# Optimization experiments

Hardware: AMD Instinct MI355X
Metric: run time of the kernel (lower is better)

## Reference

```python
import jax, jax.numpy as jnp
import numpy as np

FEATURE_DIM = 4
LOSS_WEIGHT = 1.0
DELTA_V = 0.5
DELTA_D = 1.5
NUM_LABELS = 8  # instance ids 0..7; 0 = background
B, H, W = 16, 640, 640


def _safe_norm(x, axis):
    # L2 norm with grad-safe sqrt (forward value exact: 0 when sum of squares is 0)
    sq = jnp.sum(x * x, axis=axis)
    pos = sq > 0
    return jnp.where(pos, jnp.sqrt(jnp.where(pos, sq, 1.0)), 0.0)


def _single_loss(emb, instance, kernel, training_mask):
    # emb: [H,W,C], instance: [H,W] int, kernel/training_mask: [H,W] float
    C = emb.shape[-1]
    L = NUM_LABELS
    tm = training_mask > 0.5
    kr = kernel > 0.5
    inst = jnp.where(tm, instance, 0).reshape(-1)          # [P]
    inst_k = jnp.where(kr.reshape(-1), inst, 0)            # [P]
    emb_f = emb.reshape(-1, C)                              # [P,C]

    # per-label kernel-region means (emb_mean), label 0 column is zeros
    sums = jax.ops.segment_sum(emb_f, inst_k, num_segments=L)                       # [L,C]
    cnts = jax.ops.segment_sum(jnp.ones(inst_k.shape, jnp.float32), inst_k, L)      # [L]
    mu = sums / jnp.maximum(cnts, 1.0)[:, None]
    mu = mu.at[0].set(0.0)

    # aggregation term: per-pixel distance to its instance mean
    d = _safe_norm(emb_f - mu[inst], axis=1)                                         # [P]
    term = jnp.log(jnp.maximum(d - DELTA_V, 0.0) ** 2 + 1.0)
    cnt_i = jax.ops.segment_sum(jnp.ones(inst.shape, jnp.float32), inst, L)
    agg = jax.ops.segment_sum(term, inst, L) / jnp.maximum(cnt_i, 1.0)               # [L]
    # original skips label 0, then takes mean of l_agg[1:] -> drops first nonzero label
    l_agg = jnp.mean(agg[2:])

    # discrimination term: all ordered pairs of distinct nonzero labels
    dd = _safe_norm(mu[:, None, :] - mu[None, :, :], axis=-1)                        # [L,L]
    valid = (1.0 - jnp.eye(L, dtype=jnp.float32)).at[0, :].set(0.0).at[:, 0].set(0.0)
    dis = jnp.log(jnp.maximum(2.0 * DELTA_D - dd, 0.0) ** 2 + 1.0)
    l_dis = jnp.sum(dis * valid) / jnp.sum(valid)

    l_reg = jnp.mean(jnp.log(_safe_norm(mu, axis=1) + 1.0)) * 0.001
    return l_agg + l_dis + l_reg


def reference(emb, instance, kernel, training_mask):
    losses = jax.vmap(_single_loss)(emb, instance, kernel, training_mask)  # [B]
    return LOSS_WEIGHT * jnp.mean(losses)


def setup_inputs() -> dict:
    key = jax.random.key(0)
    k1, k2, k3 = jax.random.split(key, 3)
    emb = jax.random.normal(k1, (B, H, W, FEATURE_DIM), dtype=jnp.float32)
    instance = jax.random.randint(k2, (B, H, W), 0, NUM_LABELS, dtype=jnp.int32)
    kernel = jax.random.uniform(k3, (B, H, W), dtype=jnp.float32)
    training_mask = jnp.ones((B, H, W), dtype=jnp.float32)
    return {"emb": emb, "instance": instance, "kernel": kernel, "training_mask": training_mask}
```

## Files before the change

kernel.cpp:

```cpp
#include <hip/hip_runtime.h>
#include <math.h>

#define NLAB 8
#define BATCH 16
#define S_OFF  0
#define CK_OFF 28
#define CI_OFF 35
#define AG_OFF 41
#define ACC_PER_B 48
#define ACC_FLOATS (BATCH * ACC_PER_B)
#define LAB_OFFSET 4096
#define GX_ACC 64
#define GX_AGG 96
#define ILP 8

typedef __attribute__((ext_vector_type(2))) float v2f;

__device__ __forceinline__ v2f v2fma(v2f a, v2f b, v2f c) {
#if defined(__has_builtin) && __has_builtin(__builtin_elementwise_fma)
  return __builtin_elementwise_fma(a, b, c);
#else
  v2f r; r.x = fmaf(a.x, b.x, c.x); r.y = fmaf(a.y, b.y, c.y); return r;
#endif
}

__device__ __forceinline__ float wave_reduce(float v) {
#pragma unroll
  for (int off = 32; off > 0; off >>= 1) v += __shfl_xor(v, off, 64);
  return v;
}

__global__ __launch_bounds__(256, 4) void k_accum(
    const float4* __restrict__ emb, const int* __restrict__ inst,
    const float* __restrict__ ker, const float* __restrict__ tmk,
    float* __restrict__ acc, unsigned char* __restrict__ labc,
    int P, int use_cache)
{
  const int b = blockIdx.y;
  const size_t base = (size_t)b * P;
  const float4* e  = emb + base;
  const int*    ip = inst + base;
  const float*  kp = ker + base;
  const float*  tp = tmk + base;
  unsigned char* lb = labc + base;

  v2f s2[7][2], cnt2[7];
#pragma unroll
  for (int j = 0; j < 7; ++j) {
    s2[j][0] = (v2f)(0.f);
    s2[j][1] = (v2f)(0.f);
    cnt2[j]  = (v2f)(0.f);
  }

  const int T   = blockDim.x * gridDim.x;
  const int tid = blockIdx.x * blockDim.x + threadIdx.x;

  int p0 = tid;
  for (; p0 + (ILP - 1) * T < P; p0 += ILP * T) {
    int   iv[ILP]; float tv[ILP], kv[ILP]; float4 ev[ILP];
#pragma unroll
    for (int k = 0; k < ILP; ++k) iv[k] = ip[p0 + k * T];
#pragma unroll
    for (int k = 0; k < ILP; ++k) tv[k] = tp[p0 + k * T];
#pragma unroll
    for (int k = 0; k < ILP; ++k) kv[k] = kp[p0 + k * T];
#pragma unroll
    for (int k = 0; k < ILP; ++k) ev[k] = e[p0 + k * T];
    __builtin_amdgcn_sched_barrier(0);

    int lab[ILP]; float kf[ILP];
#pragma unroll
    for (int k = 0; k < ILP; ++k) {
      lab[k] = (tv[k] > 0.5f) ? (iv[k] & 7) : 0;
      kf[k]  = (kv[k] > 0.5f) ? 1.f : 0.f;
      if (use_cache) lb[p0 + k * T] = (unsigned char)lab[k];
    }

#pragma unroll
    for (int l = 1; l < NLAB; ++l) {
#pragma unroll
      for (int k = 0; k < ILP; ++k) {
        float m  = (lab[k] == l) ? 1.f : 0.f;
        float mk = m * kf[k];
        v2f mk2; mk2.x = mk; mk2.y = mk;
        v2f e01; e01.x = ev[k].x; e01.y = ev[k].y;
        v2f e23; e23.x = ev[k].z; e23.y = ev[k].w;
        v2f cm;  cm.x = mk; cm.y = m;
        s2[l - 1][0] = v2fma(mk2, e01, s2[l - 1][0]);
        s2[l - 1][1] = v2fma(mk2, e23, s2[l - 1][1]);
        cnt2[l - 1] += cm;
      }
    }
  }
  for (int p = p0; p < P; p += T) {
    int   iv = ip[p];
    float tv = tp[p];
    float kv = kp[p];
    float4 ev = e[p];
    int lab = (tv > 0.5f) ? (iv & 7) : 0;
    float kf = (kv > 0.5f) ? 1.f : 0.f;
    if (use_cache) lb[p] = (unsigned char)lab;
#pragma unroll
    for (int l = 1; l < NLAB; ++l) {
      float m  = (lab == l) ? 1.f : 0.f;
      float mk = m * kf;
      v2f mk2; mk2.x = mk; mk2.y = mk;
      v2f e01; e01.x = ev.x; e01.y = ev.y;
      v2f e23; e23.x = ev.z; e23.y = ev.w;
      v2f cm;  cm.x = mk; cm.y = m;
      s2[l - 1][0] = v2fma(mk2, e01, s2[l - 1][0]);
      s2[l - 1][1] = v2fma(mk2, e23, s2[l - 1][1]);
      cnt2[l - 1] += cm;
    }
  }

  __shared__ float red[4][48];
  const int wid = threadIdx.x >> 6, lane = threadIdx.x & 63;
#pragma unroll
  for (int j = 0; j < 7; ++j) {
    float v0 = wave_reduce(s2[j][0].x);
    float v1 = wave_reduce(s2[j][0].y);
    float v2 = wave_reduce(s2[j][1].x);
    float v3 = wave_reduce(s2[j][1].y);
    float vk = wave_reduce(cnt2[j].x);
    if (lane == 0) {
      red[wid][S_OFF + j * 4 + 0] = v0;
      red[wid][S_OFF + j * 4 + 1] = v1;
      red[wid][S_OFF + j * 4 + 2] = v2;
      red[wid][S_OFF + j * 4 + 3] = v3;
      red[wid][CK_OFF + j] = vk;
    }
    if (j >= 1) {
      float vi = wave_reduce(cnt2[j].y);
      if (lane == 0) red[wid][CI_OFF + (j - 1)] = vi;
    }
  }
  __syncthreads();
  if (threadIdx.x < AG_OFF) {
    float v = red[0][threadIdx.x] + red[1][threadIdx.x] +
              red[2][threadIdx.x] + red[3][threadIdx.x];
    atomicAdd(acc + b * ACC_PER_B + threadIdx.x, v);
  }
}

__global__ __launch_bounds__(256, 6) void k_agg(
    const float4* __restrict__ emb, const int* __restrict__ inst,
    const float* __restrict__ tmk, const unsigned char* __restrict__ labc,
    float* __restrict__ acc, int P, int use_cache)
{
  const int b = blockIdx.y;
  const size_t base = (size_t)b * P;
  __shared__ float4 smu[NLAB];
  const float* accB = acc + b * ACC_PER_B;
  if (threadIdx.x < NLAB) {
    int l = threadIdx.x;
    float4 m;
    if (l == 0) {
      m = make_float4(0.f, 0.f, 0.f, 0.f);
    } else {
      float inv = 1.f / fmaxf(accB[CK_OFF + l - 1], 1.f);
      m = make_float4(accB[S_OFF + (l - 1) * 4 + 0] * inv,
                      accB[S_OFF + (l - 1) * 4 + 1] * inv,
                      accB[S_OFF + (l - 1) * 4 + 2] * inv,
                      accB[S_OFF + (l - 1) * 4 + 3] * inv);
    }
    smu[l] = m;
  }
  __syncthreads();

  const float4* e = emb + base;
  const unsigned char* lb = labc + base;
  const int*   ip = inst + base;
  const float* tp = tmk + base;

  float aggl[6];
#pragma unroll
  for (int l = 0; l < 6; ++l) aggl[l] = 0.f;

  const int T   = blockDim.x * gridDim.x;
  const int tid = blockIdx.x * blockDim.x + threadIdx.x;

  int p0 = tid;
  for (; p0 + (ILP - 1) * T < P; p0 += ILP * T) {
    int lab[ILP]; float4 ev[ILP];
    if (use_cache) {
#pragma unroll
      for (int k = 0; k < ILP; ++k) lab[k] = lb[p0 + k * T];
    } else {
      int iv[ILP]; float tv[ILP];
#pragma unroll
      for (int k = 0; k < ILP; ++k) iv[k] = ip[p0 + k * T];
#pragma unroll
      for (int k = 0; k < ILP; ++k) tv[k] = tp[p0 + k * T];
#pragma unroll
      for (int k = 0; k < ILP; ++k) lab[k] = (tv[k] > 0.5f) ? (iv[k] & 7) : 0;
    }
#pragma unroll
    for (int k = 0; k < ILP; ++k) ev[k] = e[p0 + k * T];
    __builtin_amdgcn_sched_barrier(0);

#pragma unroll
    for (int k = 0; k < ILP; ++k) {
      float4 mv = smu[lab[k]];
      float dx = ev[k].x - mv.x, dy = ev[k].y - mv.y;
      float dz = ev[k].z - mv.z, dw = ev[k].w - mv.w;
      float sq = dx * dx + dy * dy + dz * dz + dw * dw;
      float d  = sqrtf(sq);
      float t  = fmaxf(d - 0.5f, 0.f);
      float term = (lab[k] >= 2) ? logf(fmaf(t, t, 1.f)) : 0.f;
#pragma unroll
      for (int l = 0; l < 6; ++l) aggl[l] += (lab[k] == l + 2) ? term : 0.f;
    }
  }
  for (int p = p0; p < P; p += T) {
    int lab;
    if (use_cache) lab = lb[p];
    else           lab = (tp[p] > 0.5f) ? (ip[p] & 7) : 0;
    float4 ev = e[p];
    float4 mv = smu[lab];
    float dx = ev.x - mv.x, dy = ev.y - mv.y;
    float dz = ev.z - mv.z, dw = ev.w - mv.w;
    float d = sqrtf(dx * dx + dy * dy + dz * dz + dw * dw);
    float t = fmaxf(d - 0.5f, 0.f);
    float term = (lab >= 2) ? logf(fmaf(t, t, 1.f)) : 0.f;
#pragma unroll
    for (int l = 0; l < 6; ++l) aggl[l] += (lab == l + 2) ? term : 0.f;
  }

  __shared__ float red[4][8];
  const int wid = threadIdx.x >> 6, lane = threadIdx.x & 63;
#pragma unroll
  for (int l = 0; l < 6; ++l) {
    float v = wave_reduce(aggl[l]);
    if (lane == 0) red[wid][l] = v;
  }
  __syncthreads();
  if (threadIdx.x < 6) {
    float v = red[0][threadIdx.x] + red[1][threadIdx.x] +
              red[2][threadIdx.x] + red[3][threadIdx.x];
    atomicAdd(acc + b * ACC_PER_B + AG_OFF + threadIdx.x, v);
  }
}

__global__ void k_final(const float* __restrict__ acc, float* __restrict__ out, int nb) {
  const int lane = threadIdx.x;
  float loss = 0.f;
  if (lane < nb) {
    const float* a = acc + lane * ACC_PER_B;
    float mu[NLAB][4];
#pragma unroll
    for (int c = 0; c < 4; ++c) mu[0][c] = 0.f;
#pragma unroll
    for (int l = 1; l < NLAB; ++l) {
      float inv = 1.f / fmaxf(a[CK_OFF + l - 1], 1.f);
#pragma unroll
      for (int c = 0; c < 4; ++c) mu[l][c] = a[S_OFF + (l - 1) * 4 + c] * inv;
    }
    float l_agg = 0.f;
#pragma unroll
    for (int l = 2; l < NLAB; ++l)
      l_agg += a[AG_OFF + l - 2] / fmaxf(a[CI_OFF + l - 2], 1.f);
    l_agg *= (1.f / 6.f);
    float ssum = 0.f;
    for (int i = 1; i < NLAB; ++i)
      for (int j = 1; j < NLAB; ++j) {
        if (i == j) continue;
        float dx = mu[i][0] - mu[j][0], dy = mu[i][1] - mu[j][1];
        float dz = mu[i][2] - mu[j][2], dw = mu[i][3] - mu[j][3];
        float dd = sqrtf(dx * dx + dy * dy + dz * dz + dw * dw);
        float t = fmaxf(3.0f - dd, 0.f);
        ssum += logf(fmaf(t, t, 1.f));
      }
    float l_dis = ssum / 42.f;
    float rsum = 0.f;
#pragma unroll
    for (int l = 1; l < NLAB; ++l) {
      float n = sqrtf(mu[l][0] * mu[l][0] + mu[l][1] * mu[l][1] +
                      mu[l][2] * mu[l][2] + mu[l][3] * mu[l][3]);
      rsum += logf(n + 1.f);
    }
    float l_reg = rsum * (0.001f / NLAB);
    loss = l_agg + l_dis + l_reg;
  }
  loss = wave_reduce(loss);
  if (lane == 0) out[0] = loss / (float)nb;
}

extern "C" void kernel_launch(void* const* d_in, const int* in_sizes, int n_in,
                              void* d_out, int out_size, void* d_ws, size_t ws_size,
                              hipStream_t stream) {
  const float4* emb = (const float4*)d_in[0];
  const int*    inst = (const int*)d_in[1];
  const float*  ker  = (const float*)d_in[2];
  const float*  tmk  = (const float*)d_in[3];
  float* out = (float*)d_out;

  const int total = in_sizes[1];
  const int P = total / BATCH;

  float* acc = (float*)d_ws;
  unsigned char* labc = (unsigned char*)((char*)d_ws + LAB_OFFSET);
  const size_t need = (size_t)LAB_OFFSET + (size_t)total;
  const int use_cache = (ws_size >= need) ? 1 : 0;

  hipMemsetAsync(d_ws, 0, ACC_FLOATS * sizeof(float), stream);

  k_accum<<<dim3(GX_ACC, BATCH), 256, 0, stream>>>(emb, inst, ker, tmk, acc, labc, P, use_cache);
  k_agg  <<<dim3(GX_AGG, BATCH), 256, 0, stream>>>(emb, inst, tmk, labc, acc, P, use_cache);
  k_final<<<1, 64, 0, stream>>>(acc, out, BATCH);
}
```

Before: 241.6 us.

## Pack per-label counts into 64-bit byte counters and retune grid/ILP

```diff
diff --git a/kernel.cpp b/kernel.cpp
--- a/kernel.cpp
+++ b/kernel.cpp
@@ -10,11 +10,11 @@
 #define ACC_PER_B 48
 #define ACC_FLOATS (BATCH * ACC_PER_B)
 #define LAB_OFFSET 4096
-#define GX_ACC 64
-#define GX_AGG 96
-#define ILP 8
+#define GX 128
+#define ILP 4
 
 typedef __attribute__((ext_vector_type(2))) float v2f;
+typedef unsigned long long ull;
 
 __device__ __forceinline__ v2f v2fma(v2f a, v2f b, v2f c) {
 #if defined(__has_builtin) && __has_builtin(__builtin_elementwise_fma)
@@ -29,8 +29,13 @@
   for (int off = 32; off > 0; off >>= 1) v += __shfl_xor(v, off, 64);
   return v;
 }
-
-__global__ __launch_bounds__(256, 4) void k_accum(
+__device__ __forceinline__ ull wr64(ull v) {
+#pragma unroll
+  for (int off = 32; off > 0; off >>= 1) v += __shfl_xor(v, off, 64);
+  return v;
+}
+
+__global__ __launch_bounds__(256, 8) void k_accum(
     const float4* __restrict__ emb, const int* __restrict__ inst,
     const float* __restrict__ ker, const float* __restrict__ tmk,
     float* __restrict__ acc, unsigned char* __restrict__ labc,
@@ -44,13 +49,10 @@
   const float*  tp = tmk + base;
   unsigned char* lb = labc + base;
 
-  v2f s2[7][2], cnt2[7];
-#pragma unroll
-  for (int j = 0; j < 7; ++j) {
-    s2[j][0] = (v2f)(0.f);
-    s2[j][1] = (v2f)(0.f);
-    cnt2[j]  = (v2f)(0.f);
-  }
+  v2f s2[7][2];
+#pragma unroll
+  for (int j = 0; j < 7; ++j) { s2[j][0] = (v2f)(0.f); s2[j][1] = (v2f)(0.f); }
+  ull ck64 = 0, ci64 = 0;
 
   const int T   = blockDim.x * gridDim.x;
   const int tid = blockIdx.x * blockDim.x + threadIdx.x;
@@ -66,29 +68,23 @@
     for (int k = 0; k < ILP; ++k) kv[k] = kp[p0 + k * T];
 #pragma unroll
     for (int k = 0; k < ILP; ++k) ev[k] = e[p0 + k * T];
-    __builtin_amdgcn_sched_barrier(0);
-
-    int lab[ILP]; float kf[ILP];
+
 #pragma unroll
     for (int k = 0; k < ILP; ++k) {
-      lab[k] = (tv[k] > 0.5f) ? (iv[k] & 7) : 0;
-      kf[k]  = (kv[k] > 0.5f) ? 1.f : 0.f;
-      if (use_cache) lb[p0 + k * T] = (unsigned char)lab[k];
-    }
-
-#pragma unroll
-    for (int l = 1; l < NLAB; ++l) {
-#pragma unroll
-      for (int k = 0; k < ILP; ++k) {
-        float m  = (lab[k] == l) ? 1.f : 0.f;
-        float mk = m * kf[k];
+      int lab = (tv[k] > 0.5f) ? (iv[k] & 7) : 0;
+      int ki  = (kv[k] > 0.5f) ? 1 : 0;
+      float kf = (float)ki;
+      if (use_cache) lb[p0 + k * T] = (unsigned char)lab;
+      ci64 += 1ull << (8 * lab);
+      ck64 += (ull)ki << (8 * lab);
+#pragma unroll
+      for (int l = 1; l < NLAB; ++l) {
+        float mk = (lab == l) ? kf : 0.f;
         v2f mk2; mk2.x = mk; mk2.y = mk;
         v2f e01; e01.x = ev[k].x; e01.y = ev[k].y;
         v2f e23; e23.x = ev[k].z; e23.y = ev[k].w;
-        v2f cm;  cm.x = mk; cm.y = m;
         s2[l - 1][0] = v2fma(mk2, e01, s2[l - 1][0]);
         s2[l - 1][1] = v2fma(mk2, e23, s2[l - 1][1]);
-        cnt2[l - 1] += cm;
       }
     }
   }
@@ -98,19 +94,19 @@
     float kv = kp[p];
     float4 ev = e[p];
     int lab = (tv > 0.5f) ? (iv & 7) : 0;
-    float kf = (kv > 0.5f) ? 1.f : 0.f;
+    int ki  = (kv > 0.5f) ? 1 : 0;
+    float kf = (float)ki;
     if (use_cache) lb[p] = (unsigned char)lab;
+    ci64 += 1ull << (8 * lab);
+    ck64 += (ull)ki << (8 * lab);
 #pragma unroll
     for (int l = 1; l < NLAB; ++l) {
-      float m  = (lab == l) ? 1.f : 0.f;
-      float mk = m * kf;
+      float mk = (lab == l) ? kf : 0.f;
       v2f mk2; mk2.x = mk; mk2.y = mk;
       v2f e01; e01.x = ev.x; e01.y = ev.y;
       v2f e23; e23.x = ev.z; e23.y = ev.w;
-      v2f cm;  cm.x = mk; cm.y = m;
       s2[l - 1][0] = v2fma(mk2, e01, s2[l - 1][0]);
       s2[l - 1][1] = v2fma(mk2, e23, s2[l - 1][1]);
-      cnt2[l - 1] += cm;
     }
   }
 
@@ -122,17 +118,30 @@
     float v1 = wave_reduce(s2[j][0].y);
     float v2 = wave_reduce(s2[j][1].x);
     float v3 = wave_reduce(s2[j][1].y);
-    float vk = wave_reduce(cnt2[j].x);
     if (lane == 0) {
       red[wid][S_OFF + j * 4 + 0] = v0;
       red[wid][S_OFF + j * 4 + 1] = v1;
       red[wid][S_OFF + j * 4 + 2] = v2;
       red[wid][S_OFF + j * 4 + 3] = v3;
-      red[wid][CK_OFF + j] = vk;
-    }
-    if (j >= 1) {
-      float vi = wave_reduce(cnt2[j].y);
-      if (lane == 0) red[wid][CI_OFF + (j - 1)] = vi;
+    }
+  }
+  {
+    const ull M8 = 0x00FF00FF00FF00FFull;
+    ull ckA = wr64(ck64 & M8);
+    ull ckB = wr64((ck64 >> 8) & M8);
+    ull ciA = wr64(ci64 & M8);
+    ull ciB = wr64((ci64 >> 8) & M8);
+    if (lane == 0) {
+#pragma unroll
+      for (int l = 1; l < NLAB; ++l) {
+        ull v = (l & 1) ? (ckB >> (16 * (l >> 1))) : (ckA >> (16 * (l >> 1)));
+        red[wid][CK_OFF + l - 1] = (float)(v & 0xFFFF);
+      }
+#pragma unroll
+      for (int l = 2; l < NLAB; ++l) {
+        ull v = (l & 1) ? (ciB >> (16 * (l >> 1))) : (ciA >> (16 * (l >> 1)));
+        red[wid][CI_OFF + l - 2] = (float)(v & 0xFFFF);
+      }
     }
   }
   __syncthreads();
@@ -143,7 +152,7 @@
   }
 }
 
-__global__ __launch_bounds__(256, 6) void k_agg(
+__global__ __launch_bounds__(256, 8) void k_agg(
     const float4* __restrict__ emb, const int* __restrict__ inst,
     const float* __restrict__ tmk, const unsigned char* __restrict__ labc,
     float* __restrict__ acc, int P, int use_cache)
@@ -197,7 +206,6 @@
     }
 #pragma unroll
     for (int k = 0; k < ILP; ++k) ev[k] = e[p0 + k * T];
-    __builtin_amdgcn_sched_barrier(0);
 
 #pragma unroll
     for (int k = 0; k < ILP; ++k) {
@@ -305,7 +313,7 @@
 
   hipMemsetAsync(d_ws, 0, ACC_FLOATS * sizeof(float), stream);
 
-  k_accum<<<dim3(GX_ACC, BATCH), 256, 0, stream>>>(emb, inst, ker, tmk, acc, labc, P, use_cache);
-  k_agg  <<<dim3(GX_AGG, BATCH), 256, 0, stream>>>(emb, inst, tmk, labc, acc, P, use_cache);
+  k_accum<<<dim3(GX, BATCH), 256, 0, stream>>>(emb, inst, ker, tmk, acc, labc, P, use_cache);
+  k_agg  <<<dim3(GX, BATCH), 256, 0, stream>>>(emb, inst, tmk, labc, acc, P, use_cache);
   k_final<<<1, 64, 0, stream>>>(acc, out, BATCH);
 }
```

After: 255.0 us. 5.5% more time.
